# Optimization experiments

Measured on AMD Instinct MI355X. Metric: run time of the kernel, lower is better.

Reference implementation:

```python
import jax, jax.numpy as jnp
import numpy as np

B, L, D, H, NL = 32, 200, 64, 2, 2
ITEM_NUM, TIME_SPAN = 50000, 365
NEG = float(-2**32 + 1)


def _ln(x, g, b, eps=1e-8):
    m = jnp.mean(x, -1, keepdims=True)
    v = jnp.mean((x - m) ** 2, -1, keepdims=True)
    return (x - m) / jnp.sqrt(v + eps) * g + b


def setup_inputs() -> dict:
    key = jax.random.key(0)
    ks = iter(jax.random.split(key, 32))
    f = lambda shape: jax.random.normal(next(ks), shape, jnp.float32) * 0.02
    item_emb = f((ITEM_NUM + 1, D)).at[0].set(0.0)  # padding_idx=0
    return dict(
        log_ids=jax.random.randint(next(ks), (B, L), 0, ITEM_NUM + 1),
        log_times=jax.random.randint(next(ks), (B, L), 0, 100_000_000),
        pos_ids=jax.random.randint(next(ks), (B, L), 1, ITEM_NUM + 1),
        neg_ids=jax.random.randint(next(ks), (B, L), 1, ITEM_NUM + 1),
        item_emb=item_emb,
        posK_emb=f((L, D)), posV_emb=f((L, D)),
        tK_emb=f((TIME_SPAN + 1, D)), tV_emb=f((TIME_SPAN + 1, D)),
        ln1_g=jnp.ones((NL, D)), ln1_b=jnp.zeros((NL, D)),
        Wq=f((NL, D, D)), bq=jnp.zeros((NL, D)),
        Wk=f((NL, D, D)), bk=jnp.zeros((NL, D)),
        Wv=f((NL, D, D)), bv=jnp.zeros((NL, D)),
        ln2_g=jnp.ones((NL, D)), ln2_b=jnp.zeros((NL, D)),
        W1=f((NL, D, D)), b1=jnp.zeros((NL, D)),
        W2=f((NL, D, D)), b2=jnp.zeros((NL, D)),
        lnf_g=jnp.ones((D,)), lnf_b=jnp.zeros((D,)),
    )


def _attention(xq, xkv, pad, cmask, tK, tV, pK, pV, Wq, bq, Wk, bk, Wv, bv):
    dh = D // H
    Q = xq @ Wq.T + bq
    K = xkv @ Wk.T + bk
    V = xkv @ Wv.T + bv
    heads = lambda t: t.reshape(B, L, H, dh).transpose(2, 0, 1, 3)  # [H,B,L,dh]
    Qh, Kh, Vh = heads(Q), heads(K), heads(V)
    pKh = pK.reshape(L, H, dh).transpose(1, 0, 2)  # [H,L,dh] (same for all b)
    pVh = pV.reshape(L, H, dh).transpose(1, 0, 2)
    tKh = tK.reshape(B, L, L, H, dh).transpose(3, 0, 1, 2, 4)  # [H,B,Lq,Lk,dh]
    tVh = tV.reshape(B, L, L, H, dh).transpose(3, 0, 1, 2, 4)
    s = jnp.einsum('hbqd,hbkd->hbqk', Qh, Kh)
    s = s + jnp.einsum('hbqd,hkd->hbqk', Qh, pKh)
    s = s + jnp.einsum('hbqkd,hbqd->hbqk', tKh, Qh)
    s = s / (dh ** 0.5)
    s = jnp.where(pad[None, :, :, None], NEG, s)  # padded query rows
    s = jnp.where(cmask[None, None, :, :], NEG, s)  # causal mask
    A = jax.nn.softmax(s, axis=-1)
    out = jnp.einsum('hbqk,hbkd->hbqd', A, Vh)
    out = out + jnp.einsum('hbqk,hkd->hbqd', A, pVh)
    out = out + jnp.einsum('hbqk,hbqkd->hbqd', A, tVh)
    return out.transpose(1, 2, 0, 3).reshape(B, L, D)


def reference(log_ids, log_times, pos_ids, neg_ids, item_emb, posK_emb, posV_emb,
              tK_emb, tV_emb, ln1_g, ln1_b, Wq, bq, Wk, bk, Wv, bv,
              ln2_g, ln2_b, W1, b1, W2, b2, lnf_g, lnf_b):
    # per-pair time-interval buckets (days, clipped to TIME_SPAN)
    dt = jnp.abs(log_times[:, :, None] - log_times[:, None, :]).astype(jnp.float32) / 86400.0
    tmat = jnp.minimum(dt, TIME_SPAN).astype(jnp.int32)
    tK = tK_emb[tmat]  # [B,L,L,D]
    tV = tV_emb[tmat]
    pad = (log_ids == 0)
    keep = (~pad)[:, :, None].astype(item_emb.dtype)
    cmask = ~jnp.tril(jnp.ones((L, L), dtype=bool))
    x = item_emb[log_ids] * (D ** 0.5) * keep
    for i in range(NL):
        q = _ln(x, ln1_g[i], ln1_b[i])
        mha = _attention(q, x, pad, cmask, tK, tV, posK_emb, posV_emb,
                         Wq[i], bq[i], Wk[i], bk[i], Wv[i], bv[i])
        x = q + mha
        x = _ln(x, ln2_g[i], ln2_b[i])
        x = x + (jax.nn.relu(x @ W1[i].T + b1[i]) @ W2[i].T + b2[i])  # 1x1 conv FFN
        x = x * keep
    feats = _ln(x, lnf_g, lnf_b)
    pos_logits = jnp.sum(feats * item_emb[pos_ids], -1)
    neg_logits = jnp.sum(feats * item_emb[neg_ids], -1)
    return pos_logits, neg_logits
```

## Files before the change

kernel.cpp:

```cpp
#include <hip/hip_runtime.h>
#include <math.h>

#define BB 32
#define LLEN 200
#define DD 64
#define HH 2
#define NLAYER 2
#define BLD (BB * LLEN * DD)
#define TSPAN1 366

__device__ inline float waveSum(float v) {
#pragma unroll
    for (int off = 32; off > 0; off >>= 1) v += __shfl_xor(v, off);
    return v;
}
__device__ inline float halfSum(float v) {
    v += __shfl_xor(v, 1);
    v += __shfl_xor(v, 2);
    v += __shfl_xor(v, 4);
    v += __shfl_xor(v, 8);
    v += __shfl_xor(v, 16);
    return v;
}
__device__ inline float halfMax(float v) {
    v = fmaxf(v, __shfl_xor(v, 1));
    v = fmaxf(v, __shfl_xor(v, 2));
    v = fmaxf(v, __shfl_xor(v, 4));
    v = fmaxf(v, __shfl_xor(v, 8));
    v = fmaxf(v, __shfl_xor(v, 16));
    return v;
}

__global__ void transpose_kernel(const float* __restrict__ Wq,
                                 const float* __restrict__ Wk,
                                 const float* __restrict__ Wv,
                                 const float* __restrict__ W1,
                                 const float* __restrict__ W2,
                                 const float* __restrict__ tK_emb,
                                 float* __restrict__ wt,
                                 float* __restrict__ tKT) {
    int m = blockIdx.x;
    if (m < 10) {
        const float* src;
        switch (m % 5) {
            case 0: src = Wq; break;
            case 1: src = Wk; break;
            case 2: src = Wv; break;
            case 3: src = W1; break;
            default: src = W2; break;
        }
        src += (m / 5) * DD * DD;
        float* dst = wt + m * DD * DD;
        for (int e = threadIdx.x; e < DD * DD; e += 256) {
            int d = e >> 6, j = e & 63;
            dst[j * DD + d] = src[e];
        }
    } else {
        for (int e = threadIdx.x; e < TSPAN1 * DD; e += 256) {
            int t = e >> 6, d = e & 63;
            tKT[d * TSPAN1 + t] = tK_emb[e];
        }
    }
}

__global__ void embed_kernel(const int* __restrict__ log_ids,
                             const float* __restrict__ item_emb,
                             float* __restrict__ x) {
    int tid = threadIdx.x;
    int row = blockIdx.x * 4 + (tid >> 6);
    int d = tid & 63;
    int id = log_ids[row];
    float v = item_emb[id * DD + d] * 8.0f;
    x[row * DD + d] = (id == 0) ? 0.0f : v;
}

__global__ void ln_qkv_kernel(const float* __restrict__ x,
                              const float* __restrict__ g,
                              const float* __restrict__ bln,
                              const float* __restrict__ WqT, const float* __restrict__ bq,
                              const float* __restrict__ WkT, const float* __restrict__ bk,
                              const float* __restrict__ WvT, const float* __restrict__ bv,
                              const float* __restrict__ posK,
                              const float* __restrict__ posV,
                              float* __restrict__ q,
                              float* __restrict__ Q, float* __restrict__ K,
                              float* __restrict__ V) {
    __shared__ float qs[4][DD], xs[4][DD];
    int tid = threadIdx.x;
    int wid = tid >> 6, d = tid & 63;
    int row = blockIdx.x * 4 + wid;
    int l = row % LLEN;
    float xv = x[row * DD + d];
    xs[wid][d] = xv;
    float m = waveSum(xv) * (1.0f / 64.0f);
    float c = xv - m;
    float var = waveSum(c * c) * (1.0f / 64.0f);
    float qv = (c / sqrtf(var + 1e-8f)) * g[d] + bln[d];
    qs[wid][d] = qv;
    q[row * DD + d] = qv;
    float aq = bq[d], ak = bk[d], av = bv[d];
#pragma unroll 8
    for (int j = 0; j < DD; ++j) {
        aq = fmaf(qs[wid][j], WqT[j * DD + d], aq);
        ak = fmaf(xs[wid][j], WkT[j * DD + d], ak);
        av = fmaf(xs[wid][j], WvT[j * DD + d], av);
    }
    Q[row * DD + d] = aq;
    K[row * DD + d] = ak + posK[l * DD + d];
    V[row * DD + d] = av + posV[l * DD + d];
}

__global__ void qt_kernel(const float* __restrict__ Q,
                          const float* __restrict__ tKT,
                          float* __restrict__ Qt_g) {
    __shared__ float Qs[8][DD];
    int tid = threadIdx.x;
    int base = blockIdx.x * 8;
    for (int e = tid; e < 8 * DD; e += 384)
        Qs[e >> 6][e & 63] = Q[(base + (e >> 6)) * DD + (e & 63)];
    __syncthreads();
    int t = tid;
    if (t < TSPAN1) {
        float accA[8] = {0, 0, 0, 0, 0, 0, 0, 0};
        float accB[8] = {0, 0, 0, 0, 0, 0, 0, 0};
        for (int d = 0; d < 32; ++d) {
            float v = tKT[d * TSPAN1 + t];
#pragma unroll
            for (int gg = 0; gg < 8; ++gg) accA[gg] = fmaf(v, Qs[gg][d], accA[gg]);
        }
        for (int d = 32; d < 64; ++d) {
            float v = tKT[d * TSPAN1 + t];
#pragma unroll
            for (int gg = 0; gg < 8; ++gg) accB[gg] = fmaf(v, Qs[gg][d], accB[gg]);
        }
#pragma unroll
        for (int gg = 0; gg < 8; ++gg) {
            Qt_g[(base + gg) * (2 * TSPAN1) + t] = accA[gg];
            Qt_g[(base + gg) * (2 * TSPAN1) + TSPAN1 + t] = accB[gg];
        }
    }
}

__global__ void attn_kernel(const float* __restrict__ Q,
                            const float* __restrict__ Keff,
                            const float* __restrict__ Veff,
                            const int* __restrict__ log_times,
                            const float* __restrict__ Qt_g,
                            const float* __restrict__ tV_emb,
                            float* __restrict__ out) {
    __shared__ int t_s[LLEN];
    __shared__ float sc[4][HH][LLEN];
    __shared__ unsigned short tm_s[4][LLEN];
    __shared__ float qt_s[4][2 * TSPAN1];

    int tid = threadIdx.x;
    int wid = tid >> 6;
    int lane = tid & 63;
    int bi = blockIdx.x / 50;
    int i = blockIdx.x % 50;
    int qi = (wid == 0) ? i : (wid == 1) ? (99 - i) : (wid == 2) ? (100 + i) : (199 - i);
    int row = bi * LLEN + qi;
    int len = qi + 1;

    if (tid < LLEN) t_s[tid] = log_times[bi * LLEN + tid];
    __syncthreads();

    const float* qtrow = Qt_g + row * (2 * TSPAN1);
    for (int e = lane; e < 2 * TSPAN1; e += 64) qt_s[wid][e] = qtrow[e];

    int tq = t_s[qi];
    for (int k = lane; k < len; k += 64) {
        int dt = tq - t_s[k];
        if (dt < 0) dt = -dt;
        float dtf = fminf((float)dt * (1.0f / 86400.0f), 365.0f);
        tm_s[wid][k] = (unsigned short)(int)dtf;
    }

    int h = lane >> 5;
    int l5 = lane & 31;
    int cch = l5 >> 2;
    int j = l5 & 3;
    float4 qv = ((const float4*)(Q + row * DD))[h * 8 + cch];
    const float4* K4 = (const float4*)(Keff + bi * LLEN * DD);
    const float scale = 0.17677669529663687f;

    for (int k0 = 0; k0 < len; k0 += 4) {
        int k = k0 + j;
        int kc = (k < len) ? k : (len - 1);
        int bucket = tm_s[wid][kc];
        float4 kv = K4[kc * 16 + h * 8 + cch];
        float p = qv.x * kv.x + qv.y * kv.y + qv.z * kv.z + qv.w * kv.w;
        p += __shfl_xor(p, 4);
        p += __shfl_xor(p, 8);
        p += __shfl_xor(p, 16);
        float s = (p + qt_s[wid][h * TSPAN1 + bucket]) * scale;
        if (cch == 0 && k < len) sc[wid][h][k] = s;
    }

    {
        int kl = l5;
        float m = -INFINITY;
        for (int k = kl; k < len; k += 32) m = fmaxf(m, sc[wid][h][k]);
        m = halfMax(m);
        float s = 0.0f;
        for (int k = kl; k < len; k += 32) {
            float e = expf(sc[wid][h][k] - m);
            sc[wid][h][k] = e;
            s += e;
        }
        s = halfSum(s);
        float inv = 1.0f / s;
        for (int k = kl; k < len; k += 32) sc[wid][h][k] *= inv;
    }

    const float* Vb = Veff + bi * LLEN * DD + lane;
    const float* tVl = tV_emb + lane;
    float acc0 = 0.0f, acc1 = 0.0f, acc2 = 0.0f, acc3 = 0.0f;
    int k = 0;
    for (; k + 4 <= len; k += 4) {
        int b0 = tm_s[wid][k + 0];
        int b1 = tm_s[wid][k + 1];
        int b2 = tm_s[wid][k + 2];
        int b3 = tm_s[wid][k + 3];
        float a0 = sc[wid][h][k + 0];
        float a1 = sc[wid][h][k + 1];
        float a2 = sc[wid][h][k + 2];
        float a3 = sc[wid][h][k + 3];
        acc0 = fmaf(a0, Vb[(k + 0) * DD] + tVl[b0 * DD], acc0);
        acc1 = fmaf(a1, Vb[(k + 1) * DD] + tVl[b1 * DD], acc1);
        acc2 = fmaf(a2, Vb[(k + 2) * DD] + tVl[b2 * DD], acc2);
        acc3 = fmaf(a3, Vb[(k + 3) * DD] + tVl[b3 * DD], acc3);
    }
    for (; k < len; ++k) {
        int b0 = tm_s[wid][k];
        acc0 = fmaf(sc[wid][h][k], Vb[k * DD] + tVl[b0 * DD], acc0);
    }
    out[row * DD + lane] = (acc0 + acc1) + (acc2 + acc3);
}

__global__ void addln_ffn_kernel(const float* __restrict__ qin,
                                 const float* __restrict__ att,
                                 const float* __restrict__ g,
                                 const float* __restrict__ bln,
                                 const float* __restrict__ W1T, const float* __restrict__ b1,
                                 const float* __restrict__ W2T, const float* __restrict__ b2,
                                 const int* __restrict__ log_ids,
                                 float* __restrict__ xout) {
    __shared__ float xs[4][DD], hs[4][DD];
    int tid = threadIdx.x;
    int wid = tid >> 6, d = tid & 63;
    int row = blockIdx.x * 4 + wid;
    float v = qin[row * DD + d] + att[row * DD + d];
    float m = waveSum(v) * (1.0f / 64.0f);
    float c = v - m;
    float var = waveSum(c * c) * (1.0f / 64.0f);
    float xv = (c / sqrtf(var + 1e-8f)) * g[d] + bln[d];
    xs[wid][d] = xv;
    float a = b1[d];
#pragma unroll 8
    for (int j = 0; j < DD; ++j) a = fmaf(xs[wid][j], W1T[j * DD + d], a);
    hs[wid][d] = fmaxf(a, 0.0f);
    float o = b2[d];
#pragma unroll 8
    for (int j = 0; j < DD; ++j) o = fmaf(hs[wid][j], W2T[j * DD + d], o);
    float res = xv + o;
    if (log_ids[row] == 0) res = 0.0f;
    xout[row * DD + d] = res;
}

__global__ void final_kernel(const float* __restrict__ x,
                             const float* __restrict__ g,
                             const float* __restrict__ b,
                             const float* __restrict__ item_emb,
                             const int* __restrict__ pos_ids,
                             const int* __restrict__ neg_ids,
                             float* __restrict__ out) {
    int tid = threadIdx.x;
    int wid = tid >> 6, d = tid & 63;
    int row = blockIdx.x * 4 + wid;
    float v = x[row * DD + d];
    float m = waveSum(v) * (1.0f / 64.0f);
    float c = v - m;
    float var = waveSum(c * c) * (1.0f / 64.0f);
    float f = (c / sqrtf(var + 1e-8f)) * g[d] + b[d];
    int pid = pos_ids[row];
    int nid = neg_ids[row];
    float p = waveSum(f * item_emb[pid * DD + d]);
    float n = waveSum(f * item_emb[nid * DD + d]);
    if (d == 0) {
        out[row] = p;
        out[BB * LLEN + row] = n;
    }
}

extern "C" void kernel_launch(void* const* d_in, const int* in_sizes, int n_in,
                              void* d_out, int out_size, void* d_ws, size_t ws_size,
                              hipStream_t stream) {
    const int* log_ids = (const int*)d_in[0];
    const int* log_times = (const int*)d_in[1];
    const int* pos_ids = (const int*)d_in[2];
    const int* neg_ids = (const int*)d_in[3];
    const float* item_emb = (const float*)d_in[4];
    const float* posK = (const float*)d_in[5];
    const float* posV = (const float*)d_in[6];
    const float* tK_emb = (const float*)d_in[7];
    const float* tV_emb = (const float*)d_in[8];
    const float* ln1_g = (const float*)d_in[9];
    const float* ln1_b = (const float*)d_in[10];
    const float* Wq = (const float*)d_in[11];
    const float* bq = (const float*)d_in[12];
    const float* Wk = (const float*)d_in[13];
    const float* bk = (const float*)d_in[14];
    const float* Wv = (const float*)d_in[15];
    const float* bv = (const float*)d_in[16];
    const float* ln2_g = (const float*)d_in[17];
    const float* ln2_b = (const float*)d_in[18];
    const float* W1 = (const float*)d_in[19];
    const float* b1 = (const float*)d_in[20];
    const float* W2 = (const float*)d_in[21];
    const float* b2 = (const float*)d_in[22];
    const float* lnf_g = (const float*)d_in[23];
    const float* lnf_b = (const float*)d_in[24];

    float* ws = (float*)d_ws;
    float* x = ws;
    float* q = x + BLD;
    float* Qb = q + BLD;
    float* Kb = Qb + BLD;
    float* Vb = Kb + BLD;
    float* att = Vb + BLD;
    float* wt = att + BLD;
    float* tKT = wt + 10 * DD * DD;
    float* Qt = tKT + DD * TSPAN1;

    const int nrow = BB * LLEN;

    transpose_kernel<<<11, 256, 0, stream>>>(Wq, Wk, Wv, W1, W2, tK_emb, wt, tKT);
    embed_kernel<<<nrow / 4, 256, 0, stream>>>(log_ids, item_emb, x);

    for (int i = 0; i < NLAYER; ++i) {
        const float* WqT = wt + (i * 5 + 0) * DD * DD;
        const float* WkT = wt + (i * 5 + 1) * DD * DD;
        const float* WvT = wt + (i * 5 + 2) * DD * DD;
        const float* W1T = wt + (i * 5 + 3) * DD * DD;
        const float* W2T = wt + (i * 5 + 4) * DD * DD;
        ln_qkv_kernel<<<nrow / 4, 256, 0, stream>>>(x, ln1_g + i * DD, ln1_b + i * DD,
                                                    WqT, bq + i * DD,
                                                    WkT, bk + i * DD,
                                                    WvT, bv + i * DD,
                                                    posK, posV,
                                                    q, Qb, Kb, Vb);
        qt_kernel<<<nrow / 8, 384, 0, stream>>>(Qb, tKT, Qt);
        attn_kernel<<<BB * 50, 256, 0, stream>>>(Qb, Kb, Vb, log_times,
                                                 Qt, tV_emb, att);
        addln_ffn_kernel<<<nrow / 4, 256, 0, stream>>>(q, att, ln2_g + i * DD,
                                                       ln2_b + i * DD,
                                                       W1T, b1 + i * DD,
                                                       W2T, b2 + i * DD,
                                                       log_ids, x);
    }

    final_kernel<<<nrow / 4, 256, 0, stream>>>(x, lnf_g, lnf_b, item_emb,
                                               pos_ids, neg_ids, (float*)d_out);
}
```

Before: 196.9 us.

## Fuse embedding into first LN-QKV, widen qt tile, pair queries per attention wave

Folds the embedding gather into the first layer's LN/QKV kernel, which removes one launch and one pass over the activations. The time-projection kernel now handles 16 rows per block instead of 8, so each tKT load is reused across more query rows. The attention kernel gives each wave two complementary causal rows (j and 199-j). They share K and V loads and the per-wave work is balanced, and the Qt rows are read straight from global memory instead of being staged in shared memory. This halves the attention grid and raises register pressure, which may lower occupancy.

```diff
diff --git a/kernel.cpp b/kernel.cpp
--- a/kernel.cpp
+++ b/kernel.cpp
@@ -63,18 +63,10 @@
     }
 }
 
-__global__ void embed_kernel(const int* __restrict__ log_ids,
-                             const float* __restrict__ item_emb,
-                             float* __restrict__ x) {
-    int tid = threadIdx.x;
-    int row = blockIdx.x * 4 + (tid >> 6);
-    int d = tid & 63;
-    int id = log_ids[row];
-    float v = item_emb[id * DD + d] * 8.0f;
-    x[row * DD + d] = (id == 0) ? 0.0f : v;
-}
-
 __global__ void ln_qkv_kernel(const float* __restrict__ x,
+                              const int* __restrict__ log_ids,
+                              const float* __restrict__ item_emb,
+                              int first,
                               const float* __restrict__ g,
                               const float* __restrict__ bln,
                               const float* __restrict__ WqT, const float* __restrict__ bq,
@@ -90,7 +82,13 @@
     int wid = tid >> 6, d = tid & 63;
     int row = blockIdx.x * 4 + wid;
     int l = row % LLEN;
-    float xv = x[row * DD + d];
+    float xv;
+    if (first) {
+        int id = log_ids[row];
+        xv = (id == 0) ? 0.0f : item_emb[id * DD + d] * 8.0f;
+    } else {
+        xv = x[row * DD + d];
+    }
     xs[wid][d] = xv;
     float m = waveSum(xv) * (1.0f / 64.0f);
     float c = xv - m;
@@ -113,31 +111,35 @@
 __global__ void qt_kernel(const float* __restrict__ Q,
                           const float* __restrict__ tKT,
                           float* __restrict__ Qt_g) {
-    __shared__ float Qs[8][DD];
+    __shared__ float Qs[16][DD];
     int tid = threadIdx.x;
-    int base = blockIdx.x * 8;
-    for (int e = tid; e < 8 * DD; e += 384)
+    int base = blockIdx.x * 16;
+    for (int e = tid; e < 16 * DD; e += 384)
         Qs[e >> 6][e & 63] = Q[(base + (e >> 6)) * DD + (e & 63)];
     __syncthreads();
     int t = tid;
     if (t < TSPAN1) {
-        float accA[8] = {0, 0, 0, 0, 0, 0, 0, 0};
-        float accB[8] = {0, 0, 0, 0, 0, 0, 0, 0};
+        float acc[16];
+#pragma unroll
+        for (int gg = 0; gg < 16; ++gg) acc[gg] = 0.0f;
         for (int d = 0; d < 32; ++d) {
             float v = tKT[d * TSPAN1 + t];
 #pragma unroll
-            for (int gg = 0; gg < 8; ++gg) accA[gg] = fmaf(v, Qs[gg][d], accA[gg]);
-        }
+            for (int gg = 0; gg < 16; ++gg) acc[gg] = fmaf(v, Qs[gg][d], acc[gg]);
+        }
+#pragma unroll
+        for (int gg = 0; gg < 16; ++gg)
+            Qt_g[(base + gg) * (2 * TSPAN1) + t] = acc[gg];
+#pragma unroll
+        for (int gg = 0; gg < 16; ++gg) acc[gg] = 0.0f;
         for (int d = 32; d < 64; ++d) {
             float v = tKT[d * TSPAN1 + t];
 #pragma unroll
-            for (int gg = 0; gg < 8; ++gg) accB[gg] = fmaf(v, Qs[gg][d], accB[gg]);
-        }
-#pragma unroll
-        for (int gg = 0; gg < 8; ++gg) {
-            Qt_g[(base + gg) * (2 * TSPAN1) + t] = accA[gg];
-            Qt_g[(base + gg) * (2 * TSPAN1) + TSPAN1 + t] = accB[gg];
-        }
+            for (int gg = 0; gg < 16; ++gg) acc[gg] = fmaf(v, Qs[gg][d], acc[gg]);
+        }
+#pragma unroll
+        for (int gg = 0; gg < 16; ++gg)
+            Qt_g[(base + gg) * (2 * TSPAN1) + TSPAN1 + t] = acc[gg];
     }
 }
 
@@ -149,93 +151,128 @@
                             const float* __restrict__ tV_emb,
                             float* __restrict__ out) {
     __shared__ int t_s[LLEN];
-    __shared__ float sc[4][HH][LLEN];
-    __shared__ unsigned short tm_s[4][LLEN];
-    __shared__ float qt_s[4][2 * TSPAN1];
+    __shared__ float sc[4][2][HH][LLEN];
+    __shared__ unsigned short tm[4][2][LLEN];
 
     int tid = threadIdx.x;
     int wid = tid >> 6;
     int lane = tid & 63;
-    int bi = blockIdx.x / 50;
-    int i = blockIdx.x % 50;
-    int qi = (wid == 0) ? i : (wid == 1) ? (99 - i) : (wid == 2) ? (100 + i) : (199 - i);
-    int row = bi * LLEN + qi;
-    int len = qi + 1;
+    int bi = blockIdx.x / 25;
+    int j = (blockIdx.x % 25) * 4 + wid;
+    int qa = j, qb = 199 - j;
+    int rowa = bi * LLEN + qa, rowb = bi * LLEN + qb;
+    int lena = qa + 1, lenb = qb + 1;
 
     if (tid < LLEN) t_s[tid] = log_times[bi * LLEN + tid];
     __syncthreads();
 
-    const float* qtrow = Qt_g + row * (2 * TSPAN1);
-    for (int e = lane; e < 2 * TSPAN1; e += 64) qt_s[wid][e] = qtrow[e];
-
-    int tq = t_s[qi];
-    for (int k = lane; k < len; k += 64) {
-        int dt = tq - t_s[k];
-        if (dt < 0) dt = -dt;
-        float dtf = fminf((float)dt * (1.0f / 86400.0f), 365.0f);
-        tm_s[wid][k] = (unsigned short)(int)dtf;
+    {
+        int tqa = t_s[qa], tqb = t_s[qb];
+        for (int k = lane; k < lenb; k += 64) {
+            int tk = t_s[k];
+            int dta = tqa - tk; if (dta < 0) dta = -dta;
+            int dtb = tqb - tk; if (dtb < 0) dtb = -dtb;
+            if (k < lena)
+                tm[wid][0][k] = (unsigned short)(int)fminf((float)dta * (1.0f / 86400.0f), 365.0f);
+            tm[wid][1][k] = (unsigned short)(int)fminf((float)dtb * (1.0f / 86400.0f), 365.0f);
+        }
     }
 
     int h = lane >> 5;
     int l5 = lane & 31;
     int cch = l5 >> 2;
-    int j = l5 & 3;
-    float4 qv = ((const float4*)(Q + row * DD))[h * 8 + cch];
+    int jo = l5 & 3;
+    float4 qva = ((const float4*)(Q + rowa * DD))[h * 8 + cch];
+    float4 qvb = ((const float4*)(Q + rowb * DD))[h * 8 + cch];
     const float4* K4 = (const float4*)(Keff + bi * LLEN * DD);
+    const float* qta = Qt_g + rowa * (2 * TSPAN1) + h * TSPAN1;
+    const float* qtb = Qt_g + rowb * (2 * TSPAN1) + h * TSPAN1;
     const float scale = 0.17677669529663687f;
 
-    for (int k0 = 0; k0 < len; k0 += 4) {
-        int k = k0 + j;
-        int kc = (k < len) ? k : (len - 1);
-        int bucket = tm_s[wid][kc];
-        float4 kv = K4[kc * 16 + h * 8 + cch];
-        float p = qv.x * kv.x + qv.y * kv.y + qv.z * kv.z + qv.w * kv.w;
-        p += __shfl_xor(p, 4);
-        p += __shfl_xor(p, 8);
-        p += __shfl_xor(p, 16);
-        float s = (p + qt_s[wid][h * TSPAN1 + bucket]) * scale;
-        if (cch == 0 && k < len) sc[wid][h][k] = s;
-    }
-
-    {
-        int kl = l5;
+    int k0 = 0;
+    for (; k0 < lena; k0 += 4) {
+        int k = k0 + jo;
+        int ka = (k < lena) ? k : (lena - 1);
+        int kb = (k < lenb) ? k : (lenb - 1);
+        int ba = tm[wid][0][ka], bb2 = tm[wid][1][kb];
+        float4 kva = K4[ka * 16 + h * 8 + cch];
+        float4 kvb = K4[kb * 16 + h * 8 + cch];
+        float pa = qva.x * kva.x + qva.y * kva.y + qva.z * kva.z + qva.w * kva.w;
+        float pb = qvb.x * kvb.x + qvb.y * kvb.y + qvb.z * kvb.z + qvb.w * kvb.w;
+        pa += __shfl_xor(pa, 4);  pb += __shfl_xor(pb, 4);
+        pa += __shfl_xor(pa, 8);  pb += __shfl_xor(pb, 8);
+        pa += __shfl_xor(pa, 16); pb += __shfl_xor(pb, 16);
+        float sa = (pa + qta[ba]) * scale;
+        float sb = (pb + qtb[bb2]) * scale;
+        if (cch == 0) {
+            if (k < lena) sc[wid][0][h][k] = sa;
+            if (k < lenb) sc[wid][1][h][k] = sb;
+        }
+    }
+    for (; k0 < lenb; k0 += 4) {
+        int k = k0 + jo;
+        int kb = (k < lenb) ? k : (lenb - 1);
+        int bb2 = tm[wid][1][kb];
+        float4 kvb = K4[kb * 16 + h * 8 + cch];
+        float pb = qvb.x * kvb.x + qvb.y * kvb.y + qvb.z * kvb.z + qvb.w * kvb.w;
+        pb += __shfl_xor(pb, 4);
+        pb += __shfl_xor(pb, 8);
+        pb += __shfl_xor(pb, 16);
+        float sb = (pb + qtb[bb2]) * scale;
+        if (cch == 0 && k < lenb) sc[wid][1][h][k] = sb;
+    }
+
+#pragma unroll
+    for (int qsel = 0; qsel < 2; ++qsel) {
+        int len = qsel ? lenb : lena;
+        float* srow = sc[wid][qsel][h];
         float m = -INFINITY;
-        for (int k = kl; k < len; k += 32) m = fmaxf(m, sc[wid][h][k]);
+        for (int k = l5; k < len; k += 32) m = fmaxf(m, srow[k]);
         m = halfMax(m);
         float s = 0.0f;
-        for (int k = kl; k < len; k += 32) {
-            float e = expf(sc[wid][h][k] - m);
-            sc[wid][h][k] = e;
+        for (int k = l5; k < len; k += 32) {
+            float e = expf(srow[k] - m);
+            srow[k] = e;
             s += e;
         }
         s = halfSum(s);
         float inv = 1.0f / s;
-        for (int k = kl; k < len; k += 32) sc[wid][h][k] *= inv;
+        for (int k = l5; k < len; k += 32) srow[k] *= inv;
     }
 
     const float* Vb = Veff + bi * LLEN * DD + lane;
     const float* tVl = tV_emb + lane;
-    float acc0 = 0.0f, acc1 = 0.0f, acc2 = 0.0f, acc3 = 0.0f;
+    float aA0 = 0, aA1 = 0, aA2 = 0, aA3 = 0;
+    float aB0 = 0, aB1 = 0, aB2 = 0, aB3 = 0;
     int k = 0;
-    for (; k + 4 <= len; k += 4) {
-        int b0 = tm_s[wid][k + 0];
-        int b1 = tm_s[wid][k + 1];
-        int b2 = tm_s[wid][k + 2];
-        int b3 = tm_s[wid][k + 3];
-        float a0 = sc[wid][h][k + 0];
-        float a1 = sc[wid][h][k + 1];
-        float a2 = sc[wid][h][k + 2];
-        float a3 = sc[wid][h][k + 3];
-        acc0 = fmaf(a0, Vb[(k + 0) * DD] + tVl[b0 * DD], acc0);
-        acc1 = fmaf(a1, Vb[(k + 1) * DD] + tVl[b1 * DD], acc1);
-        acc2 = fmaf(a2, Vb[(k + 2) * DD] + tVl[b2 * DD], acc2);
-        acc3 = fmaf(a3, Vb[(k + 3) * DD] + tVl[b3 * DD], acc3);
-    }
-    for (; k < len; ++k) {
-        int b0 = tm_s[wid][k];
-        acc0 = fmaf(sc[wid][h][k], Vb[k * DD] + tVl[b0 * DD], acc0);
-    }
-    out[row * DD + lane] = (acc0 + acc1) + (acc2 + acc3);
+    for (; k + 4 <= lena; k += 4) {
+        float v0 = Vb[(k + 0) * DD], v1 = Vb[(k + 1) * DD];
+        float v2 = Vb[(k + 2) * DD], v3 = Vb[(k + 3) * DD];
+        aA0 = fmaf(sc[wid][0][h][k + 0], v0 + tVl[tm[wid][0][k + 0] * DD], aA0);
+        aB0 = fmaf(sc[wid][1][h][k + 0], v0 + tVl[tm[wid][1][k + 0] * DD], aB0);
+        aA1 = fmaf(sc[wid][0][h][k + 1], v1 + tVl[tm[wid][0][k + 1] * DD], aA1);
+        aB1 = fmaf(sc[wid][1][h][k + 1], v1 + tVl[tm[wid][1][k + 1] * DD], aB1);
+        aA2 = fmaf(sc[wid][0][h][k + 2], v2 + tVl[tm[wid][0][k + 2] * DD], aA2);
+        aB2 = fmaf(sc[wid][1][h][k + 2], v2 + tVl[tm[wid][1][k + 2] * DD], aB2);
+        aA3 = fmaf(sc[wid][0][h][k + 3], v3 + tVl[tm[wid][0][k + 3] * DD], aA3);
+        aB3 = fmaf(sc[wid][1][h][k + 3], v3 + tVl[tm[wid][1][k + 3] * DD], aB3);
+    }
+    for (; k < lena; ++k) {
+        float vv = Vb[k * DD];
+        aA0 = fmaf(sc[wid][0][h][k], vv + tVl[tm[wid][0][k] * DD], aA0);
+        aB0 = fmaf(sc[wid][1][h][k], vv + tVl[tm[wid][1][k] * DD], aB0);
+    }
+    for (; k + 4 <= lenb; k += 4) {
+        aB0 = fmaf(sc[wid][1][h][k + 0], Vb[(k + 0) * DD] + tVl[tm[wid][1][k + 0] * DD], aB0);
+        aB1 = fmaf(sc[wid][1][h][k + 1], Vb[(k + 1) * DD] + tVl[tm[wid][1][k + 1] * DD], aB1);
+        aB2 = fmaf(sc[wid][1][h][k + 2], Vb[(k + 2) * DD] + tVl[tm[wid][1][k + 2] * DD], aB2);
+        aB3 = fmaf(sc[wid][1][h][k + 3], Vb[(k + 3) * DD] + tVl[tm[wid][1][k + 3] * DD], aB3);
+    }
+    for (; k < lenb; ++k)
+        aB0 = fmaf(sc[wid][1][h][k], Vb[k * DD] + tVl[tm[wid][1][k] * DD], aB0);
+
+    out[rowa * DD + lane] = (aA0 + aA1) + (aA2 + aA3);
+    out[rowb * DD + lane] = (aB0 + aB1) + (aB2 + aB3);
 }
 
 __global__ void addln_ffn_kernel(const float* __restrict__ qin,
@@ -336,7 +373,6 @@
     const int nrow = BB * LLEN;
 
     transpose_kernel<<<11, 256, 0, stream>>>(Wq, Wk, Wv, W1, W2, tK_emb, wt, tKT);
-    embed_kernel<<<nrow / 4, 256, 0, stream>>>(log_ids, item_emb, x);
 
     for (int i = 0; i < NLAYER; ++i) {
         const float* WqT = wt + (i * 5 + 0) * DD * DD;
@@ -344,14 +380,15 @@
         const float* WvT = wt + (i * 5 + 2) * DD * DD;
         const float* W1T = wt + (i * 5 + 3) * DD * DD;
         const float* W2T = wt + (i * 5 + 4) * DD * DD;
-        ln_qkv_kernel<<<nrow / 4, 256, 0, stream>>>(x, ln1_g + i * DD, ln1_b + i * DD,
+        ln_qkv_kernel<<<nrow / 4, 256, 0, stream>>>(x, log_ids, item_emb, (i == 0),
+                                                    ln1_g + i * DD, ln1_b + i * DD,
                                                     WqT, bq + i * DD,
                                                     WkT, bk + i * DD,
                                                     WvT, bv + i * DD,
                                                     posK, posV,
                                                     q, Qb, Kb, Vb);
-        qt_kernel<<<nrow / 8, 384, 0, stream>>>(Qb, tKT, Qt);
-        attn_kernel<<<BB * 50, 256, 0, stream>>>(Qb, Kb, Vb, log_times,
+        qt_kernel<<<nrow / 16, 384, 0, stream>>>(Qb, tKT, Qt);
+        attn_kernel<<<BB * 25, 256, 0, stream>>>(Qb, Kb, Vb, log_times,
                                                  Qt, tV_emb, att);
         addln_ffn_kernel<<<nrow / 4, 256, 0, stream>>>(q, att, ln2_g + i * DD,
                                                        ln2_b + i * DD,
```

Result: slower. 224.8 us (+14.2%).
